# Performance work log

Measured on AMD Instinct MI355X. Metric: run time of the kernel, lower is better.

Reference implementation:

```python
import jax, jax.numpy as jnp
import numpy as np
from jax import lax

EPS = 1e-6
K1D = 3  # DACA conv1d kernel size for C=64


def binquant(x):
    # forward of BinaryQuantize_Quad (sign); STE only matters for bwd
    return jnp.sign(x)


def daca(x, w1d):
    # x: [B,C,H,W] -> per-channel sigmoid gate [B,C,1,1]
    b, c, h, w = x.shape
    flat = x.reshape(b, c, h * w)
    ch_mean = flat.mean(axis=2)
    ch_var = flat.var(axis=2, ddof=1) + EPS  # torch.var default unbiased=True
    ch_std = jnp.sqrt(ch_var)
    ch_abs = jnp.abs(flat).mean(axis=2)  # adaptive avg pool of |x|
    y = jnp.stack([ch_abs, ch_mean, ch_std], axis=1)  # [B,3,C]
    y = lax.conv_general_dilated(
        y, w1d, window_strides=(1,), padding=[(K1D // 2, K1D // 2)],
        dimension_numbers=("NCH", "OIH", "NCH"))  # [B,1,C]
    return jax.nn.sigmoid(y[:, 0, :, None, None])  # [B,C,1,1]


def hard_binary_conv(x, w):
    # scaling: mean |w| over (in,kh,kw), per out-channel, detached
    scale = jnp.mean(jnp.abs(w), axis=(1, 2, 3), keepdims=True)
    cw = jnp.clip(w, -1.0, 1.0)
    bw = lax.stop_gradient(scale * jnp.sign(w) - cw) + cw  # value=scale*sign(w), grad via clip
    return lax.conv_general_dilated(
        x, bw, window_strides=(1, 1), padding=[(1, 1), (1, 1)],
        dimension_numbers=("NCHW", "OIHW", "NCHW"))


def rprelu(x, b0, a, b1):
    y = x + b0
    y = jnp.where(y > 0, y, a[None, :, None, None] * y)  # PReLU per-channel
    return y + b1


def setup_inputs() -> dict:
    key = jax.random.key(0)
    ks = jax.random.split(key, 7)
    C = 64
    x = jax.random.normal(ks[0], (8, C, 256, 256), dtype=jnp.float32)
    w_conv = jax.random.normal(ks[1], (C, C, 3, 3), dtype=jnp.float32) * 0.1
    w1d = jax.random.normal(ks[2], (1, 3, K1D), dtype=jnp.float32) * 0.3
    b_move = jax.random.normal(ks[3], (1, C, 1, 1), dtype=jnp.float32) * 0.02
    pr_b0 = jax.random.normal(ks[4], (1, C, 1, 1), dtype=jnp.float32) * 0.02
    prelu_a = jnp.full((C,), 0.25, dtype=jnp.float32)
    pr_b1 = jax.random.normal(ks[5], (1, C, 1, 1), dtype=jnp.float32) * 0.02
    return {"x": x, "b_move": b_move, "w_conv": w_conv, "w1d": w1d,
            "pr_b0": pr_b0, "prelu_a": prelu_a, "pr_b1": pr_b1}


def reference(x, b_move, w_conv, w1d, pr_b0, prelu_a, pr_b1):
    out = x + b_move                 # LearnableBias move0
    scale = daca(out, w1d)           # [B,C,1,1] gate
    out = binquant(out)              # sign binarization of activations
    out = hard_binary_conv(out, w_conv)
    out = out * scale
    out = rprelu(out, pr_b0, prelu_a, pr_b1)
    return out + x                   # residual
```

## Files before the change

kernel.cpp:

```cpp
#include <hip/hip_runtime.h>
#include <stdint.h>

#define BB 8
#define C  64
#define H  256
#define W  256
#define HW (H*W)
#define EPSV 1e-6f

typedef unsigned long long u64;
typedef float __attribute__((ext_vector_type(4))) f32x4;

__global__ __launch_bounds__(256) void k_stats(const float* __restrict__ x,
                                               const float* __restrict__ bmove,
                                               float* __restrict__ sums ) {
  int bc = blockIdx.x;
  float bm = bmove[bc & 63];
  const f32x4* p = (const f32x4*)(x + (size_t)bc * HW);
  int t = threadIdx.x;
  float s = 0.f, s2 = 0.f, sa = 0.f;
  #pragma unroll 8
  for (int k = 0; k < 64; ++k) {
    f32x4 v = p[(k << 8) | t];
    float a0 = v.x + bm, a1 = v.y + bm, a2 = v.z + bm, a3 = v.w + bm;
    s  += a0 + a1 + a2 + a3;
    s2 += a0*a0 + a1*a1 + a2*a2 + a3*a3;
    sa += fabsf(a0) + fabsf(a1) + fabsf(a2) + fabsf(a3);
  }
  #pragma unroll
  for (int off = 32; off > 0; off >>= 1) {
    s  += __shfl_down(s,  off, 64);
    s2 += __shfl_down(s2, off, 64);
    sa += __shfl_down(sa, off, 64);
  }
  __shared__ float red[4][3];
  int wid = t >> 6;
  if ((t & 63) == 0) { red[wid][0] = s; red[wid][1] = s2; red[wid][2] = sa; }
  __syncthreads();
  if (t == 0) {
    float S  = red[0][0] + red[1][0] + red[2][0] + red[3][0];
    float S2 = red[0][1] + red[1][1] + red[2][1] + red[3][1];
    float SA = red[0][2] + red[1][2] + red[2][2] + red[3][2];
    sums[bc] = S; sums[512 + bc] = S2; sums[1024 + bc] = SA;
  }
}

__global__ __launch_bounds__(256) void k_pack(const float* __restrict__ x,
                                              const float* __restrict__ bmove,
                                              u64* __restrict__ packed) {
  int blk = blockIdx.x;
  int b   = blk >> 7;
  int rg  = blk & 127;
  int h0  = rg << 1;
  int tid = threadIdx.x;
  int wid = tid >> 6, lane = tid & 63;
  __shared__ f32x4 lds4[64 * 33];

  float bm = bmove[lane];
  int p4l = tid & 31;
  int cg  = tid >> 5;
  const size_t bbase = (size_t)b * C * HW;

  for (int tile = 0; tile < 4; ++tile) {
    int h  = h0 + (tile >> 1);
    int wb = (tile & 1) << 7;
    __syncthreads();
    #pragma unroll
    for (int cc = 0; cc < 8; ++cc) {
      int c = cg + (cc << 3);
      lds4[c * 33 + p4l] =
          *((const f32x4*)(x + bbase + (size_t)c * HW + h * W + wb) + p4l);
    }
    __syncthreads();
    u64* pdst = packed + ((size_t)(b * H + h)) * W + wb;
    #pragma unroll
    for (int k = 0; k < 8; ++k) {
      int p4i = (wid << 3) + k;
      f32x4 v = lds4[lane * 33 + p4i];
      u64 q0 = __ballot(v.x + bm > 0.f);
      u64 q1 = __ballot(v.y + bm > 0.f);
      u64 q2 = __ballot(v.z + bm > 0.f);
      u64 q3 = __ballot(v.w + bm > 0.f);
      u64 qa = (lane & 1) ? q1 : q0;
      u64 qb = (lane & 1) ? q3 : q2;
      u64 qq = (lane & 2) ? qb : qa;
      if (lane < 4) pdst[(p4i << 2) + lane] = qq;
    }
  }
}

__global__ __launch_bounds__(512) void k_gate(const float* __restrict__ sums,
                                              const float* __restrict__ w_conv,
                                              const float* __restrict__ w1d,
                                              float* __restrict__ alpha,
                                              u64* __restrict__ wsign) {
  __shared__ float stA[512], stM[512], stS[512];
  __shared__ float swv[64];
  int tid = threadIdx.x;
  {
    float s = sums[tid], s2 = sums[512 + tid], sa = sums[1024 + tid];
    const float invN = 1.f / (float)HW;
    float mean = s * invN;
    float var  = (s2 - s * s * invN) * (1.f / (float)(HW - 1)) + EPSV;
    stA[tid] = sa * invN;
    stM[tid] = mean;
    stS[tid] = sqrtf(var);
  }
  {
    int o = tid >> 3, g = tid & 7;
    const float* wo = w_conv + o * 576 + g * 72;
    float s = 0.f;
    u64 wb[9] = {0,0,0,0,0,0,0,0,0};
    #pragma unroll
    for (int i = 0; i < 8; i++) {
      #pragma unroll
      for (int tp = 0; tp < 9; tp++) {
        float v = wo[i * 9 + tp];
        s += fabsf(v);
        if (v > 0.f) wb[tp] |= (1ull << (g * 8 + i));
      }
    }
    #pragma unroll
    for (int off = 4; off > 0; off >>= 1) {
      s += __shfl_down(s, off, 8);
      #pragma unroll
      for (int tp = 0; tp < 9; tp++)
        wb[tp] |= __shfl_down(wb[tp], off, 8);
    }
    if (g == 0) {
      swv[o] = s * (1.f / 576.f);
      #pragma unroll
      for (int tp = 0; tp < 9; tp++) wsign[o * 9 + tp] = wb[tp];
    }
  }
  __syncthreads();
  int b = tid >> 6, c = tid & 63;
  float y = 0.f;
  #pragma unroll
  for (int k = 0; k < 3; k++) {
    int cc = c + k - 1;
    if (cc >= 0 && cc < 64) {
      int j = b * 64 + cc;
      y += stA[j] * w1d[0 * 3 + k] + stM[j] * w1d[1 * 3 + k] + stS[j] * w1d[2 * 3 + k];
    }
  }
  float gate = 1.f / (1.f + expf(-y));
  alpha[tid] = gate * swv[c];
}

__global__ __launch_bounds__(256) void k_conv4(const u64* __restrict__ packed,
                                               const u64* __restrict__ wsign,
                                               const float* __restrict__ alpha,
                                               const float* __restrict__ x,
                                               const float* __restrict__ pr_b0,
                                               const float* __restrict__ prelu_a,
                                               const float* __restrict__ pr_b1,
                                               float* __restrict__ out) {
  int blk = blockIdx.x;
  int b = blk >> 6, hg = blk & 63;
  int h0 = hg << 2;
  int t = threadIdx.x;
  __shared__ u64 rows[6][W];
  const u64* pb = packed + (size_t)b * H * W;
  #pragma unroll
  for (int r = 0; r < 6; ++r) {
    int hr = h0 - 1 + r;
    rows[r][t] = (hr >= 0 && hr < H) ? pb[hr * W + t] : 0ull;
  }
  __syncthreads();

  int tr = t >> 6, lane = t & 63;
  int tw = lane << 2;
  int h  = h0 + tr;
  bool rTop = (h > 0), rBot = (h < H - 1);
  u64 vm0 = (lane == 0)  ? 0ull : ~0ull;
  u64 vm5 = (lane == 63) ? 0ull : ~0ull;

  u64 nw[3][6];
  #pragma unroll
  for (int rr = 0; rr < 3; ++rr) {
    #pragma unroll
    for (int j = 0; j < 6; ++j) {
      int wi = tw - 1 + j;
      wi = (wi < 0) ? 0 : (wi > W - 1 ? W - 1 : wi);
      nw[rr][j] = rows[tr + rr][wi];
    }
  }
  int nr = 1 + (int)rTop + (int)rBot;
  float base0 = 64.f * (float)nr * ((lane == 0)  ? 2.f : 3.f);
  float base1 = 64.f * (float)nr * 3.f;
  float base3 = 64.f * (float)nr * ((lane == 63) ? 2.f : 3.f);

  size_t xoff = (size_t)b * C * HW + (size_t)h * W + tw;
  const float* al = alpha + b * 64;

  for (int o = 0; o < 64; ++o) {
    const u64* ws = wsign + o * 9;
    u64 w0=ws[0], w1=ws[1], w2=ws[2], w3=ws[3], w4=ws[4],
        w5=ws[5], w6=ws[6], w7=ws[7], w8=ws[8];
    int c0 = 0, c1 = 0, c2 = 0, c3 = 0;
    if (rTop) {
      c0 += __popcll((nw[0][0]^w0)&vm0) + __popcll(nw[0][1]^w1) + __popcll(nw[0][2]^w2);
      c1 += __popcll(nw[0][1]^w0) + __popcll(nw[0][2]^w1) + __popcll(nw[0][3]^w2);
      c2 += __popcll(nw[0][2]^w0) + __popcll(nw[0][3]^w1) + __popcll(nw[0][4]^w2);
      c3 += __popcll(nw[0][3]^w0) + __popcll(nw[0][4]^w1) + __popcll((nw[0][5]^w2)&vm5);
    }
    {
      c0 += __popcll((nw[1][0]^w3)&vm0) + __popcll(nw[1][1]^w4) + __popcll(nw[1][2]^w5);
      c1 += __popcll(nw[1][1]^w3) + __popcll(nw[1][2]^w4) + __popcll(nw[1][3]^w5);
      c2 += __popcll(nw[1][2]^w3) + __popcll(nw[1][3]^w4) + __popcll(nw[1][4]^w5);
      c3 += __popcll(nw[1][3]^w3) + __popcll(nw[1][4]^w4) + __popcll((nw[1][5]^w5)&vm5);
    }
    if (rBot) {
      c0 += __popcll((nw[2][0]^w6)&vm0) + __popcll(nw[2][1]^w7) + __popcll(nw[2][2]^w8);
      c1 += __popcll(nw[2][1]^w6) + __popcll(nw[2][2]^w7) + __popcll(nw[2][3]^w8);
      c2 += __popcll(nw[2][2]^w6) + __popcll(nw[2][3]^w7) + __popcll(nw[2][4]^w8);
      c3 += __popcll(nw[2][3]^w6) + __popcll(nw[2][4]^w7) + __popcll((nw[2][5]^w8)&vm5);
    }
    float a  = al[o];
    float b0 = pr_b0[o], pa = prelu_a[o], b1 = pr_b1[o];
    f32x4 xr = *(const f32x4*)(x + xoff + (size_t)o * HW);
    float d0 = (base0 - 2.f*(float)c0) * a + b0;
    float d1 = (base1 - 2.f*(float)c1) * a + b0;
    float d2 = (base1 - 2.f*(float)c2) * a + b0;
    float d3 = (base3 - 2.f*(float)c3) * a + b0;
    d0 = (d0 > 0.f) ? d0 : pa * d0;
    d1 = (d1 > 0.f) ? d1 : pa * d1;
    d2 = (d2 > 0.f) ? d2 : pa * d2;
    d3 = (d3 > 0.f) ? d3 : pa * d3;
    f32x4 ov;
    ov.x = d0 + b1 + xr.x;
    ov.y = d1 + b1 + xr.y;
    ov.z = d2 + b1 + xr.z;
    ov.w = d3 + b1 + xr.w;
    __builtin_nontemporal_store(ov, (f32x4*)(out + xoff + (size_t)o * HW));
  }
}

extern "C" void kernel_launch(void* const* d_in, const int* in_sizes, int n_in,
                              void* d_out, int out_size, void* d_ws, size_t ws_size,
                              hipStream_t stream) {
  const float* x       = (const float*)d_in[0];
  const float* b_move  = (const float*)d_in[1];
  const float* w_conv  = (const float*)d_in[2];
  const float* w1d     = (const float*)d_in[3];
  const float* pr_b0   = (const float*)d_in[4];
  const float* prelu_a = (const float*)d_in[5];
  const float* pr_b1   = (const float*)d_in[6];
  float* out = (float*)d_out;

  char* ws = (char*)d_ws;
  u64*   packed = (u64*)ws;
  float* sums   = (float*)(ws + 4194304);
  float* alpha  = (float*)(ws + 4194304 + 8192);
  u64*   wsign  = (u64*)(ws + 4194304 + 16384);

  k_stats<<<512, 256, 0, stream>>>(x, b_move, sums);
  k_pack<<<1024, 256, 0, stream>>>(x, b_move, packed);
  k_gate<<<1, 512, 0, stream>>>(sums, w_conv, w1d, alpha, wsign);
  k_conv4<<<512, 256, 0, stream>>>(packed, wsign, alpha, x,
                                   pr_b0, prelu_a, pr_b1, out);
}
```

Before: 120.5 us.

## Compute binary conv via int8 MFMA instead of XOR-popcount

Replaces the XOR/popcount binary convolution with int8 32x32x32 MFMA, using ±1 weight bytes and 0/1 activation bytes expanded from the packed sign bits. The gate kernel now precomputes the weight byte table and per-border weight sums so the ±1 dot product can be recovered as 2*acc - sum(w). This aims to move the inner-product work onto matrix cores, at the cost of a large LDS table load per block and scalar (non-vector) epilogue stores.

```diff
diff --git a/kernel.cpp b/kernel.cpp
--- a/kernel.cpp
+++ b/kernel.cpp
@@ -10,6 +10,8 @@
 
 typedef unsigned long long u64;
 typedef float __attribute__((ext_vector_type(4))) f32x4;
+typedef int __attribute__((ext_vector_type(4)))  v4i;
+typedef int __attribute__((ext_vector_type(16))) v16i;
 
 __global__ __launch_bounds__(256) void k_stats(const float* __restrict__ x,
                                                const float* __restrict__ bmove,
@@ -93,10 +95,36 @@
                                               const float* __restrict__ w_conv,
                                               const float* __restrict__ w1d,
                                               float* __restrict__ alpha,
-                                              u64* __restrict__ wsign) {
+                                              float* __restrict__ sumw_g,
+                                              char*  __restrict__ atab) {
   __shared__ float stA[512], stM[512], stS[512];
   __shared__ float swv[64];
+  __shared__ float stap[64][9];
   int tid = threadIdx.x;
+
+  for (int e = tid; e < 2304; e += 512) {
+    int mt = e / 1152; int rem = e - mt * 1152;
+    int ks = rem >> 6;  int l = rem & 63;
+    int o  = mt * 32 + (l & 31);
+    int st = ks & 1;    int tap = ks >> 1;
+    int c0 = st * 32 + (l >> 5) * 16;
+    unsigned q[4];
+    #pragma unroll
+    for (int qi = 0; qi < 4; ++qi) {
+      unsigned v = 0;
+      #pragma unroll
+      for (int j = 0; j < 4; ++j) {
+        int c = c0 + qi * 4 + j;
+        float wv = w_conv[o * 576 + c * 9 + tap];
+        unsigned by = (wv > 0.f) ? 0x01u : 0xFFu;
+        v |= by << (8 * j);
+      }
+      q[qi] = v;
+    }
+    v4i qv; qv.x = (int)q[0]; qv.y = (int)q[1]; qv.z = (int)q[2]; qv.w = (int)q[3];
+    *(v4i*)(atab + (size_t)e * 16) = qv;
+  }
+
   {
     float s = sums[tid], s2 = sums[512 + tid], sa = sums[1024 + tid];
     const float invN = 1.f / (float)HW;
@@ -130,10 +158,22 @@
     if (g == 0) {
       swv[o] = s * (1.f / 576.f);
       #pragma unroll
-      for (int tp = 0; tp < 9; tp++) wsign[o * 9 + tp] = wb[tp];
+      for (int tp = 0; tp < 9; tp++)
+        stap[o][tp] = (float)(2 * (int)__popcll(wb[tp]) - 64);
     }
   }
   __syncthreads();
+  for (int i = tid; i < 576; i += 512) {
+    int cse = i >> 6, o = i & 63;
+    int vc = cse / 3, hc = cse - vc * 3;
+    int ky0 = (vc == 0) ? 1 : 0, ky1 = (vc == 2) ? 1 : 2;
+    int kx0 = (hc == 0) ? 1 : 0, kx1 = (hc == 2) ? 1 : 2;
+    float sw = 0.f;
+    for (int ky = ky0; ky <= ky1; ++ky)
+      for (int kx = kx0; kx <= kx1; ++kx)
+        sw += stap[o][ky * 3 + kx];
+    sumw_g[cse * 64 + o] = sw;
+  }
   int b = tid >> 6, c = tid & 63;
   float y = 0.f;
   #pragma unroll
@@ -148,92 +188,90 @@
   alpha[tid] = gate * swv[c];
 }
 
-__global__ __launch_bounds__(256) void k_conv4(const u64* __restrict__ packed,
-                                               const u64* __restrict__ wsign,
-                                               const float* __restrict__ alpha,
-                                               const float* __restrict__ x,
-                                               const float* __restrict__ pr_b0,
-                                               const float* __restrict__ prelu_a,
-                                               const float* __restrict__ pr_b1,
-                                               float* __restrict__ out) {
+__global__ __launch_bounds__(256) void k_convmm(const u64* __restrict__ packed,
+                                                const char* __restrict__ atab,
+                                                const float* __restrict__ sumw_g,
+                                                const float* __restrict__ alpha,
+                                                const float* __restrict__ x,
+                                                const float* __restrict__ pr_b0,
+                                                const float* __restrict__ prelu_a,
+                                                const float* __restrict__ pr_b1,
+                                                float* __restrict__ out) {
   int blk = blockIdx.x;
-  int b = blk >> 6, hg = blk & 63;
-  int h0 = hg << 2;
-  int t = threadIdx.x;
-  __shared__ u64 rows[6][W];
-  const u64* pb = packed + (size_t)b * H * W;
+  int b = blk >> 9, h = (blk >> 1) & 255, wq = blk & 1;
+  int tid = threadIdx.x, wv = tid >> 6, lane = tid & 63;
+  int w0 = wq * 128 + wv * 32;
+  int px = w0 + (lane & 31);
+  int half = lane >> 5;
+
+  __shared__ v4i  s_at[2304];
+  __shared__ float s_sumw[576];
+  __shared__ float s_al[64], s_b0[64], s_pa[64], s_b1[64];
+  for (int i = tid; i < 2304; i += 256) s_at[i] = ((const v4i*)atab)[i];
+  for (int i = tid; i < 576; i += 256) s_sumw[i] = sumw_g[i];
+  if (tid < 64) {
+    s_al[tid] = alpha[b * 64 + tid];
+    s_b0[tid] = pr_b0[tid]; s_pa[tid] = prelu_a[tid]; s_b1[tid] = pr_b1[tid];
+  }
+  __syncthreads();
+
+  v16i acc0 = {0,0,0,0,0,0,0,0,0,0,0,0,0,0,0,0};
+  v16i acc1 = {0,0,0,0,0,0,0,0,0,0,0,0,0,0,0,0};
+  const u64* pb = packed + (size_t)b * HW;
+  const unsigned MAGIC = 0x00204081u;
+
   #pragma unroll
-  for (int r = 0; r < 6; ++r) {
-    int hr = h0 - 1 + r;
-    rows[r][t] = (hr >= 0 && hr < H) ? pb[hr * W + t] : 0ull;
-  }
-  __syncthreads();
-
-  int tr = t >> 6, lane = t & 63;
-  int tw = lane << 2;
-  int h  = h0 + tr;
-  bool rTop = (h > 0), rBot = (h < H - 1);
-  u64 vm0 = (lane == 0)  ? 0ull : ~0ull;
-  u64 vm5 = (lane == 63) ? 0ull : ~0ull;
-
-  u64 nw[3][6];
+  for (int dy = -1; dy <= 1; ++dy) {
+    int hh = h + dy;
+    if (hh < 0 || hh > H - 1) continue;
+    const u64* rp = pb + hh * W;
+    u64 m[3];
+    #pragma unroll
+    for (int dx = 0; dx < 3; ++dx) {
+      int wn = px + dx - 1;
+      int wc = wn < 0 ? 0 : (wn > W - 1 ? W - 1 : wn);
+      u64 mm = rp[wc];
+      m[dx] = (wn == wc) ? mm : 0ull;
+    }
+    #pragma unroll
+    for (int dx = 0; dx < 3; ++dx) {
+      int tap = (dy + 1) * 3 + dx;
+      #pragma unroll
+      for (int st = 0; st < 2; ++st) {
+        int c0 = st * 32 + half * 16;
+        unsigned n16 = (unsigned)(m[dx] >> c0) & 0xFFFFu;
+        v4i bf;
+        bf.x = (int)(((n16        & 0xFu) * MAGIC) & 0x01010101u);
+        bf.y = (int)((((n16 >> 4) & 0xFu) * MAGIC) & 0x01010101u);
+        bf.z = (int)((((n16 >> 8) & 0xFu) * MAGIC) & 0x01010101u);
+        bf.w = (int)((((n16 >>12) & 0xFu) * MAGIC) & 0x01010101u);
+        int ks = tap * 2 + st;
+        v4i a0 = s_at[ks * 64 + lane];
+        v4i a1 = s_at[(18 + ks) * 64 + lane];
+        acc0 = __builtin_amdgcn_mfma_i32_32x32x32_i8(a0, bf, acc0, 0, 0, 0);
+        acc1 = __builtin_amdgcn_mfma_i32_32x32x32_i8(a1, bf, acc1, 0, 0, 0);
+      }
+    }
+  }
+
+  int vc = (h == 0) ? 0 : ((h == H - 1) ? 2 : 1);
+  int hc = (px == 0) ? 0 : ((px == W - 1) ? 2 : 1);
+  const float* swrow = s_sumw + (vc * 3 + hc) * 64;
+  int oadd = half * 4;
+  size_t pxoff = (size_t)b * C * HW + (size_t)h * W + px;
+
   #pragma unroll
-  for (int rr = 0; rr < 3; ++rr) {
-    #pragma unroll
-    for (int j = 0; j < 6; ++j) {
-      int wi = tw - 1 + j;
-      wi = (wi < 0) ? 0 : (wi > W - 1 ? W - 1 : wi);
-      nw[rr][j] = rows[tr + rr][wi];
-    }
-  }
-  int nr = 1 + (int)rTop + (int)rBot;
-  float base0 = 64.f * (float)nr * ((lane == 0)  ? 2.f : 3.f);
-  float base1 = 64.f * (float)nr * 3.f;
-  float base3 = 64.f * (float)nr * ((lane == 63) ? 2.f : 3.f);
-
-  size_t xoff = (size_t)b * C * HW + (size_t)h * W + tw;
-  const float* al = alpha + b * 64;
-
-  for (int o = 0; o < 64; ++o) {
-    const u64* ws = wsign + o * 9;
-    u64 w0=ws[0], w1=ws[1], w2=ws[2], w3=ws[3], w4=ws[4],
-        w5=ws[5], w6=ws[6], w7=ws[7], w8=ws[8];
-    int c0 = 0, c1 = 0, c2 = 0, c3 = 0;
-    if (rTop) {
-      c0 += __popcll((nw[0][0]^w0)&vm0) + __popcll(nw[0][1]^w1) + __popcll(nw[0][2]^w2);
-      c1 += __popcll(nw[0][1]^w0) + __popcll(nw[0][2]^w1) + __popcll(nw[0][3]^w2);
-      c2 += __popcll(nw[0][2]^w0) + __popcll(nw[0][3]^w1) + __popcll(nw[0][4]^w2);
-      c3 += __popcll(nw[0][3]^w0) + __popcll(nw[0][4]^w1) + __popcll((nw[0][5]^w2)&vm5);
-    }
-    {
-      c0 += __popcll((nw[1][0]^w3)&vm0) + __popcll(nw[1][1]^w4) + __popcll(nw[1][2]^w5);
-      c1 += __popcll(nw[1][1]^w3) + __popcll(nw[1][2]^w4) + __popcll(nw[1][3]^w5);
-      c2 += __popcll(nw[1][2]^w3) + __popcll(nw[1][3]^w4) + __popcll(nw[1][4]^w5);
-      c3 += __popcll(nw[1][3]^w3) + __popcll(nw[1][4]^w4) + __popcll((nw[1][5]^w5)&vm5);
-    }
-    if (rBot) {
-      c0 += __popcll((nw[2][0]^w6)&vm0) + __popcll(nw[2][1]^w7) + __popcll(nw[2][2]^w8);
-      c1 += __popcll(nw[2][1]^w6) + __popcll(nw[2][2]^w7) + __popcll(nw[2][3]^w8);
-      c2 += __popcll(nw[2][2]^w6) + __popcll(nw[2][3]^w7) + __popcll(nw[2][4]^w8);
-      c3 += __popcll(nw[2][3]^w6) + __popcll(nw[2][4]^w7) + __popcll((nw[2][5]^w8)&vm5);
-    }
-    float a  = al[o];
-    float b0 = pr_b0[o], pa = prelu_a[o], b1 = pr_b1[o];
-    f32x4 xr = *(const f32x4*)(x + xoff + (size_t)o * HW);
-    float d0 = (base0 - 2.f*(float)c0) * a + b0;
-    float d1 = (base1 - 2.f*(float)c1) * a + b0;
-    float d2 = (base1 - 2.f*(float)c2) * a + b0;
-    float d3 = (base3 - 2.f*(float)c3) * a + b0;
-    d0 = (d0 > 0.f) ? d0 : pa * d0;
-    d1 = (d1 > 0.f) ? d1 : pa * d1;
-    d2 = (d2 > 0.f) ? d2 : pa * d2;
-    d3 = (d3 > 0.f) ? d3 : pa * d3;
-    f32x4 ov;
-    ov.x = d0 + b1 + xr.x;
-    ov.y = d1 + b1 + xr.y;
-    ov.z = d2 + b1 + xr.z;
-    ov.w = d3 + b1 + xr.w;
-    __builtin_nontemporal_store(ov, (f32x4*)(out + xoff + (size_t)o * HW));
+  for (int mt = 0; mt < 2; ++mt) {
+    #pragma unroll
+    for (int r = 0; r < 16; ++r) {
+      int o = mt * 32 + (r & 3) + 8 * (r >> 2) + oadd;
+      int a = mt ? acc1[r] : acc0[r];
+      float dot = 2.0f * (float)a - swrow[o];
+      float v = dot * s_al[o] + s_b0[o];
+      v = (v > 0.f) ? v : s_pa[o] * v;
+      v += s_b1[o] + x[pxoff + (size_t)o * HW];
+      __builtin_nontemporal_store(v, out + pxoff + (size_t)o * HW);
+    }
   }
 }
 
@@ -253,11 +291,12 @@
   u64*   packed = (u64*)ws;
   float* sums   = (float*)(ws + 4194304);
   float* alpha  = (float*)(ws + 4194304 + 8192);
-  u64*   wsign  = (u64*)(ws + 4194304 + 16384);
+  float* sumw   = (float*)(ws + 4194304 + 24576);
+  char*  atab   =         (ws + 4194304 + 32768);
 
   k_stats<<<512, 256, 0, stream>>>(x, b_move, sums);
   k_pack<<<1024, 256, 0, stream>>>(x, b_move, packed);
-  k_gate<<<1, 512, 0, stream>>>(sums, w_conv, w1d, alpha, wsign);
-  k_conv4<<<512, 256, 0, stream>>>(packed, wsign, alpha, x,
-                                   pr_b0, prelu_a, pr_b1, out);
-}
+  k_gate<<<1, 512, 0, stream>>>(sums, w_conv, w1d, alpha, sumw, atab);
+  k_convmm<<<4096, 256, 0, stream>>>(packed, atab, sumw, alpha, x,
+                                     pr_b0, prelu_a, pr_b1, out);
+}
```

After: 143.6 us. 1.19x slower.
